# Optimization experiments

Hardware: AMD Instinct MI355X
Metric: run time of the kernel (lower is better)

## Reference

```python
import jax, jax.numpy as jnp
import numpy as np

N = 50000        # nodes
E = 800000       # edges
H = 128          # in = hidden = out width
L = 4            # num_layers
BN_EPS = 1e-5


def _bn(x, g, b):
    # training-mode batch norm over the node dimension (biased variance, as torch)
    mu = jnp.mean(x, axis=0)
    var = jnp.mean((x - mu) ** 2, axis=0)
    return (x - mu) * jax.lax.rsqrt(var + BN_EPS) * g + b


def setup_inputs() -> dict:
    key = jax.random.key(0)
    ks = jax.random.split(key, 16)
    s = 0.05
    return {
        "x": jax.random.normal(ks[0], (N, H), dtype=jnp.float32),
        "edge_index": jax.random.randint(ks[1], (2, E), 0, N, dtype=jnp.int32),
        # stacked per-layer MLP params (all layers share dims H->H->H)
        "fc1_w": jax.random.normal(ks[2], (L, H, H), dtype=jnp.float32) * s,
        "fc1_b": jnp.zeros((L, H), dtype=jnp.float32),
        "bn1_g": jnp.ones((L, H), dtype=jnp.float32),
        "bn1_b": jnp.zeros((L, H), dtype=jnp.float32),
        "fc2_w": jax.random.normal(ks[3], (L, H, H), dtype=jnp.float32) * s,
        "fc2_b": jnp.zeros((L, H), dtype=jnp.float32),
        "bn2_g": jnp.ones((L, H), dtype=jnp.float32),
        "bn2_b": jnp.zeros((L, H), dtype=jnp.float32),
        # outer per-layer BatchNorm (intended one-per-GIN-layer)
        "bn3_g": jnp.ones((L, H), dtype=jnp.float32),
        "bn3_b": jnp.zeros((L, H), dtype=jnp.float32),
        # final classifier
        "fc_w": jax.random.normal(ks[4], (H, H), dtype=jnp.float32) * s,
        "fc_b": jnp.zeros((H,), dtype=jnp.float32),
    }


def reference(x, edge_index, fc1_w, fc1_b, bn1_g, bn1_b, fc2_w, fc2_b,
              bn2_g, bn2_b, bn3_g, bn3_b, fc_w, fc_b):
    src = edge_index[0]
    dst = edge_index[1]
    for i in range(L):
        # GINConv, eps=0: h = MLP((1+eps)*x + sum_{j in N(v)} x_j)
        agg = jax.ops.segment_sum(x[src], dst, num_segments=N)  # [N, H]
        h = x + agg
        # MLP: relu(bn1(fc1(h))) -> bn2(fc2(.))
        h = jax.nn.relu(_bn(h @ fc1_w[i].T + fc1_b[i], bn1_g[i], bn1_b[i]))
        h = _bn(h @ fc2_w[i].T + fc2_b[i], bn2_g[i], bn2_b[i])
        # outer BN + ReLU per layer
        x = jax.nn.relu(_bn(h, bn3_g[i], bn3_b[i]))
    return x @ fc_w.T + fc_b  # [N, H]
```

## Files before the change

kernel.cpp:

```cpp
#include <hip/hip_runtime.h>

#define NN 50000
#define HD 128
#define NL 4
#define BN_EPS 1e-5f
#define NTILES 3125

typedef __attribute__((ext_vector_type(8))) short short8;
typedef __attribute__((ext_vector_type(4))) float f32x4;
typedef __attribute__((ext_vector_type(4))) uint uint4v;

__device__ inline ushort f2bf(float f){
  uint u = __float_as_uint(f);
  uint r = (u + 0x7fffu + ((u >> 16) & 1u)) >> 16;
  return (ushort)r;
}
__device__ inline float bflo(uint u){ return __uint_as_float(u << 16); }
__device__ inline float bfhi(uint u){ return __uint_as_float(u & 0xffff0000u); }
__device__ inline uint pk2(float lo, float hi){
  return (uint)f2bf(lo) | ((uint)f2bf(hi) << 16);
}

__global__ __launch_bounds__(256) void cast_all(const float* __restrict__ x,
                                                const float* __restrict__ w1,
                                                const float* __restrict__ w2,
                                                const float* __restrict__ wf,
                                                ushort* __restrict__ xb,
                                                ushort* __restrict__ wb){
  const int NX = NN * HD / 4;
  const int NT = NX + 36864;
  int i = blockIdx.x * 256 + threadIdx.x;
  int stride = gridDim.x * 256;
  for (; i < NT; i += stride){
    const float* src; ushort* dst;
    if (i < NX){ src = x + i * 4; dst = xb + i * 4; }
    else {
      int k = i - NX;
      dst = wb + k * 4;
      if (k < 16384)      src = w1 + k * 4;
      else if (k < 32768) src = w2 + (k - 16384) * 4;
      else                src = wf + (k - 32768) * 4;
    }
    float4 v = *(const float4*)src;
    ushort4 r;
    r.x = f2bf(v.x); r.y = f2bf(v.y); r.z = f2bf(v.z); r.w = f2bf(v.w);
    *(ushort4*)dst = r;
  }
}

__global__ void fill1_kernel(const int* __restrict__ dst, int* __restrict__ cnt,
                             int* __restrict__ pos, int E){
  int e = (blockIdx.x * 256 + threadIdx.x) * 4;
  if (e + 4 <= E){
    int4 d = *(const int4*)(dst + e);
    int4 p;
    p.x = atomicAdd(&cnt[d.x], 1);
    p.y = atomicAdd(&cnt[d.y], 1);
    p.z = atomicAdd(&cnt[d.z], 1);
    p.w = atomicAdd(&cnt[d.w], 1);
    *(int4*)(pos + e) = p;
  } else {
    for (; e < E; ++e) pos[e] = atomicAdd(&cnt[dst[e]], 1);
  }
}

__global__ void scan1_kernel(const int* __restrict__ deg, int* __restrict__ incl,
                             int* __restrict__ bsum, int n){
  __shared__ int tmp[1024];
  int gid = blockIdx.x * 1024 + threadIdx.x;
  int v = (gid < n) ? deg[gid] : 0;
  tmp[threadIdx.x] = v;
  __syncthreads();
  for (int ofs = 1; ofs < 1024; ofs <<= 1){
    int t = tmp[threadIdx.x];
    int a = (threadIdx.x >= ofs) ? tmp[threadIdx.x - ofs] : 0;
    __syncthreads();
    tmp[threadIdx.x] = t + a;
    __syncthreads();
  }
  if (gid < n) incl[gid] = tmp[threadIdx.x];
  if (threadIdx.x == 1023) bsum[blockIdx.x] = tmp[1023];
}

__global__ void scan2_kernel(const int* __restrict__ bsum, int* __restrict__ base,
                             int* __restrict__ off, int nb, int n){
  int lane = threadIdx.x & 63;
  int own = (lane < nb) ? bsum[lane] : 0;
  int v = own;
#pragma unroll
  for (int ofs = 1; ofs < 64; ofs <<= 1){
    int t = __shfl_up(v, ofs);
    if (lane >= ofs) v += t;
  }
  if (lane < nb) base[lane] = v - own;
  if (lane == 63) off[n] = v;
}

__global__ void scan3_kernel(const int* __restrict__ deg, const int* __restrict__ incl,
                             const int* __restrict__ base, int* __restrict__ off, int n){
  int gid = blockIdx.x * 1024 + threadIdx.x;
  if (gid < n) off[gid] = incl[gid] - deg[gid] + base[blockIdx.x];
}

__global__ void fill2_kernel(const int* __restrict__ src, const int* __restrict__ dst,
                             const int* __restrict__ off, const int* __restrict__ pos,
                             int* __restrict__ csrc, int E){
  int e = (blockIdx.x * 256 + threadIdx.x) * 4;
  if (e + 4 <= E){
    int4 d = *(const int4*)(dst + e);
    int4 p = *(const int4*)(pos + e);
    int4 s = *(const int4*)(src + e);
    csrc[off[d.x] + p.x] = s.x;
    csrc[off[d.y] + p.y] = s.y;
    csrc[off[d.z] + p.z] = s.z;
    csrc[off[d.w] + p.w] = s.w;
  } else {
    for (; e < E; ++e) csrc[off[dst[e]] + pos[e]] = src[e];
  }
}

__device__ inline void bn_params8(const float* __restrict__ st, const float* __restrict__ gA,
                                  const float* __restrict__ gB, const float* __restrict__ bB,
                                  int mode, float* sS, float* sT){
  int c = threadIdx.x;
  if (c < 128){
    float s0 = 0.f, s1 = 0.f;
#pragma unroll
    for (int k = 0; k < 8; ++k){
      s0 += st[k * 256 + c];
      s1 += st[k * 256 + 128 + c];
    }
    const float invN = 1.f / (float)NN;
    float mu = s0 * invN;
    float var = fmaxf(s1 * invN - mu * mu, 0.f);
    float S, T;
    if (mode == 0){
      S = gA[c] * rsqrtf(var + BN_EPS);
      T = gB[c] - mu * S;
    } else {
      float inv2 = rsqrtf(var + BN_EPS);
      float tt = gA[c] * inv2;
      float inv3 = rsqrtf(tt * tt * var + BN_EPS);
      S = tt * inv3 * gB[c];
      T = bB[c] - mu * S;
    }
    sS[c] = S; sT[c] = T;
  }
}

template<bool AFF>
__global__ __launch_bounds__(256) void agg_t(const ushort* __restrict__ xin,
                                             const int* __restrict__ off,
                                             const int* __restrict__ csrc,
                                             const float* __restrict__ statsIn,
                                             const float* __restrict__ g2,
                                             const float* __restrict__ g3,
                                             const float* __restrict__ b3,
                                             ushort* __restrict__ h){
  __shared__ float sS[128];
  __shared__ float sT[128];
  if (AFF){
    bn_params8(statsIn, g2, g3, b3, 1, sS, sT);
    __syncthreads();
  }
  int lane = threadIdx.x & 63;
  int grp  = lane >> 4;
  int col  = lane & 15;
  int node = blockIdx.x * 16 + (threadIdx.x >> 6) * 4 + grp;

  float S[8], T[8];
  if (AFF){
#pragma unroll
    for (int k = 0; k < 8; ++k){ S[k] = sS[col * 8 + k]; T[k] = sT[col * 8 + k]; }
  }

  const uint4v* x4 = (const uint4v*)xin;
  int s = off[node], e = off[node + 1];

  float a[8];
  {
    uint4v v = x4[node * 16 + col];
    if (AFF){
      a[0]=fmaxf(bflo(v.x)*S[0]+T[0],0.f); a[1]=fmaxf(bfhi(v.x)*S[1]+T[1],0.f);
      a[2]=fmaxf(bflo(v.y)*S[2]+T[2],0.f); a[3]=fmaxf(bfhi(v.y)*S[3]+T[3],0.f);
      a[4]=fmaxf(bflo(v.z)*S[4]+T[4],0.f); a[5]=fmaxf(bfhi(v.z)*S[5]+T[5],0.f);
      a[6]=fmaxf(bflo(v.w)*S[6]+T[6],0.f); a[7]=fmaxf(bfhi(v.w)*S[7]+T[7],0.f);
    } else {
      a[0]=bflo(v.x); a[1]=bfhi(v.x); a[2]=bflo(v.y); a[3]=bfhi(v.y);
      a[4]=bflo(v.z); a[5]=bfhi(v.z); a[6]=bflo(v.w); a[7]=bfhi(v.w);
    }
  }

#define ACC8(v)                                                                 \
  if (AFF){                                                                     \
    a[0]+=fmaxf(bflo((v).x)*S[0]+T[0],0.f); a[1]+=fmaxf(bfhi((v).x)*S[1]+T[1],0.f); \
    a[2]+=fmaxf(bflo((v).y)*S[2]+T[2],0.f); a[3]+=fmaxf(bfhi((v).y)*S[3]+T[3],0.f); \
    a[4]+=fmaxf(bflo((v).z)*S[4]+T[4],0.f); a[5]+=fmaxf(bfhi((v).z)*S[5]+T[5],0.f); \
    a[6]+=fmaxf(bflo((v).w)*S[6]+T[6],0.f); a[7]+=fmaxf(bfhi((v).w)*S[7]+T[7],0.f); \
  } else {                                                                      \
    a[0]+=bflo((v).x); a[1]+=bfhi((v).x); a[2]+=bflo((v).y); a[3]+=bfhi((v).y); \
    a[4]+=bflo((v).z); a[5]+=bfhi((v).z); a[6]+=bflo((v).w); a[7]+=bfhi((v).w); \
  }

  int j = s;
  for (; j + 4 <= e; j += 4){
    int i0 = csrc[j], i1 = csrc[j+1], i2 = csrc[j+2], i3 = csrc[j+3];
    uint4v v0 = x4[i0 * 16 + col];
    uint4v v1 = x4[i1 * 16 + col];
    uint4v v2 = x4[i2 * 16 + col];
    uint4v v3 = x4[i3 * 16 + col];
    ACC8(v0); ACC8(v1); ACC8(v2); ACC8(v3);
  }
  for (; j < e; ++j){
    uint4v v = x4[csrc[j] * 16 + col];
    ACC8(v);
  }
#undef ACC8

  uint4v o;
  o.x = pk2(a[0], a[1]); o.y = pk2(a[2], a[3]);
  o.z = pk2(a[4], a[5]); o.w = pk2(a[6], a[7]);
  __builtin_nontemporal_store(o, (uint4v*)h + node * 16 + col);
}

__global__ __launch_bounds__(512) void gemm_kernel(const ushort* __restrict__ A,
                                                   const ushort* __restrict__ W,
                                                   const float* __restrict__ bias,
                                                   ushort* __restrict__ Yb,
                                                   float* __restrict__ Yf,
                                                   float* __restrict__ statsOut,
                                                   const float* __restrict__ statsIn,
                                                   const float* __restrict__ gA,
                                                   const float* __restrict__ gB,
                                                   const float* __restrict__ bB,
                                                   int mode){
  __shared__ uint4v w4[128 * 17];
  __shared__ float ssum[128];
  __shared__ float ssq[128];
  __shared__ float sS[128];
  __shared__ float sT[128];
  const uint4v* Wg = (const uint4v*)W;
  for (int c = threadIdx.x; c < 2048; c += 512){
    w4[(c >> 4) * 17 + (c & 15)] = Wg[c];
  }
  if (statsIn) bn_params8(statsIn, gA, gB, bB, mode, sS, sT);
  if (threadIdx.x < 128){ ssum[threadIdx.x] = 0.f; ssq[threadIdx.x] = 0.f; }
  __syncthreads();

  int wave = threadIdx.x >> 6;
  int lane = threadIdx.x & 63;
  int m = lane & 15, q = lane >> 4;
  int tile = blockIdx.x * 8 + wave;
  bool tv = tile < NTILES;
  const uint4v* A4 = (const uint4v*)A;

  f32x4 acc[8];
#pragma unroll
  for (int i = 0; i < 8; ++i) acc[i] = (f32x4)0.f;

#pragma unroll
  for (int kt = 0; kt < 4; ++kt){
    short8 af = (short8)0;
    if (tv){
      uint4v t = __builtin_nontemporal_load(A4 + (tile * 16 + m) * 16 + kt * 4 + q);
      if (statsIn){
        int kc = kt * 32 + q * 8;
        uint4v pk;
        pk.x = pk2(fmaxf(bflo(t.x)*sS[kc+0]+sT[kc+0],0.f),
                   fmaxf(bfhi(t.x)*sS[kc+1]+sT[kc+1],0.f));
        pk.y = pk2(fmaxf(bflo(t.y)*sS[kc+2]+sT[kc+2],0.f),
                   fmaxf(bfhi(t.y)*sS[kc+3]+sT[kc+3],0.f));
        pk.z = pk2(fmaxf(bflo(t.z)*sS[kc+4]+sT[kc+4],0.f),
                   fmaxf(bfhi(t.z)*sS[kc+5]+sT[kc+5],0.f));
        pk.w = pk2(fmaxf(bflo(t.w)*sS[kc+6]+sT[kc+6],0.f),
                   fmaxf(bfhi(t.w)*sS[kc+7]+sT[kc+7],0.f));
        t = pk;
      }
      af = *(short8*)&t;
    }
#pragma unroll
    for (int to = 0; to < 8; ++to){
      uint4v bw = w4[(to * 16 + m) * 17 + kt * 4 + q];
      acc[to] = __builtin_amdgcn_mfma_f32_16x16x32_bf16(af, *(short8*)&bw, acc[to], 0, 0, 0);
    }
  }

  bool dost = (statsOut != nullptr);
#pragma unroll
  for (int to = 0; to < 8; ++to){
    int col = to * 16 + m;
    float bc = bias[col];
    float ls = 0.f, lq = 0.f;
    if (tv){
#pragma unroll
      for (int r = 0; r < 4; ++r){
        float v = acc[to][r] + bc;
        int row = tile * 16 + q * 4 + r;
        if (Yb) __builtin_nontemporal_store(__builtin_bit_cast(ushort, f2bf(v)), Yb + row * 128 + col);
        else    __builtin_nontemporal_store(v, Yf + row * 128 + col);
        ls += v; lq += v * v;
      }
    }
    if (dost){
      ls += __shfl_xor(ls, 16); lq += __shfl_xor(lq, 16);
      ls += __shfl_xor(ls, 32); lq += __shfl_xor(lq, 32);
      if (tv && q == 0){ atomicAdd(&ssum[col], ls); atomicAdd(&ssq[col], lq); }
    }
  }
  if (dost){
    __syncthreads();
    if (threadIdx.x < 128){
      int sb = (blockIdx.x & 7) * 256;
      atomicAdd(&statsOut[sb + threadIdx.x], ssum[threadIdx.x]);
      atomicAdd(&statsOut[sb + 128 + threadIdx.x], ssq[threadIdx.x]);
    }
  }
}

extern "C" void kernel_launch(void* const* d_in, const int* in_sizes, int n_in,
                              void* d_out, int out_size, void* d_ws, size_t ws_size,
                              hipStream_t stream) {
  const float* x     = (const float*)d_in[0];
  const int*   ei    = (const int*)d_in[1];
  const float* fc1_w = (const float*)d_in[2];
  const float* fc1_b = (const float*)d_in[3];
  const float* bn1_g = (const float*)d_in[4];
  const float* bn1_b = (const float*)d_in[5];
  const float* fc2_w = (const float*)d_in[6];
  const float* fc2_b = (const float*)d_in[7];
  const float* bn2_g = (const float*)d_in[8];
  const float* bn3_g = (const float*)d_in[10];
  const float* bn3_b = (const float*)d_in[11];
  const float* fc_w  = (const float*)d_in[12];
  const float* fc_b  = (const float*)d_in[13];

  int E = in_sizes[1] / 2;
  const int* srcp = ei;
  const int* dstp = ei + E;

  char* ws = (char*)d_ws;
  int*    off    = (int*)(ws + 0);
  int*    cnt    = (int*)(ws + 200064);
  int*    pos    = (int*)(ws + 400128);
  int*    csrc   = (int*)(ws + 3600128);
  ushort* wb     = (ushort*)(ws + 6800128);
  float*  stats  = (float*)(ws + 7095040);
  int*    sscr   = (int*)(ws + 7160576);
  ushort* xb     = (ushort*)(ws + 7161664);
  ushort* hb     = (ushort*)(ws + 19961664);
  ushort* y1b    = (ushort*)(ws + 32761664);
  ushort* y2b    = (ushort*)(ws + 45561664);

  int* incl = csrc;
  int* bsum = sscr;
  int* base = sscr + 64;

  hipMemsetAsync(cnt, 0, 200064, stream);
  hipMemsetAsync(stats, 0, 65536, stream);

  cast_all<<<2048, 256, 0, stream>>>(x, fc1_w, fc2_w, fc_w, xb, wb);

  const int EB4 = (E / 4 + 255) / 256 + 1;
  const int SB = (NN + 1023) / 1024;
  fill1_kernel<<<EB4, 256, 0, stream>>>(dstp, cnt, pos, E);
  scan1_kernel<<<SB, 1024, 0, stream>>>(cnt, incl, bsum, NN);
  scan2_kernel<<<1, 64, 0, stream>>>(bsum, base, off, SB, NN);
  scan3_kernel<<<SB, 1024, 0, stream>>>(cnt, incl, base, off, NN);
  fill2_kernel<<<EB4, 256, 0, stream>>>(srcp, dstp, off, pos, csrc, E);

  const int gb = (NTILES + 7) / 8;

  for (int i = 0; i < NL; ++i){
    if (i == 0){
      agg_t<false><<<NN / 16, 256, 0, stream>>>(xb, off, csrc,
                                                nullptr, nullptr, nullptr, nullptr, hb);
    } else {
      agg_t<true><<<NN / 16, 256, 0, stream>>>(y2b, off, csrc,
                                               stats + ((i - 1) * 2 + 1) * 2048,
                                               bn2_g + (i - 1) * 128,
                                               bn3_g + (i - 1) * 128,
                                               bn3_b + (i - 1) * 128, hb);
    }
    gemm_kernel<<<gb, 512, 0, stream>>>(hb, wb + i * 16384, fc1_b + i * 128,
                                        y1b, nullptr, stats + (i * 2) * 2048,
                                        nullptr, nullptr, nullptr, nullptr, 0);
    gemm_kernel<<<gb, 512, 0, stream>>>(y1b, wb + 65536 + i * 16384, fc2_b + i * 128,
                                        y2b, nullptr, stats + (i * 2 + 1) * 2048,
                                        stats + (i * 2) * 2048, bn1_g + i * 128,
                                        bn1_b + i * 128, nullptr, 0);
  }

  gemm_kernel<<<gb, 512, 0, stream>>>(y2b, wb + 131072, fc_b,
                                      nullptr, (float*)d_out, nullptr,
                                      stats + 7 * 2048, bn2_g + 384,
                                      bn3_g + 384, bn3_b + 384, 1);
}
```

Measured before the change: 463.7 us.

## Fuse neighbor aggregation into first MLP GEMM and use fixed-degree slot adjacency

The separate aggregation kernel is merged into the first GEMM. Each wave gathers neighbor rows for a 16-node tile into shared memory, then multiplies by fc1 with MFMA and accumulates BN statistics in the same kernel. This removes the write and re-read of the aggregated bf16 hidden matrix in every layer. The three CSR prefix-scan kernels are also replaced by a padded per-node slot array of fixed width 64, so edges are placed using only the count and position. The trade-offs are that the adjacency buffer is four times larger and that any node with more than 64 incoming edges silently overflows into the next node's slots. The fused kernel also uses more shared memory per block, which can lower occupancy for the latency-bound gather.

```diff
diff --git a/kernel.cpp b/kernel.cpp
--- a/kernel.cpp
+++ b/kernel.cpp
@@ -5,6 +5,7 @@
 #define NL 4
 #define BN_EPS 1e-5f
 #define NTILES 3125
+#define MAXDEG 64
 
 typedef __attribute__((ext_vector_type(8))) short short8;
 typedef __attribute__((ext_vector_type(4))) float f32x4;
@@ -64,58 +65,19 @@
   }
 }
 
-__global__ void scan1_kernel(const int* __restrict__ deg, int* __restrict__ incl,
-                             int* __restrict__ bsum, int n){
-  __shared__ int tmp[1024];
-  int gid = blockIdx.x * 1024 + threadIdx.x;
-  int v = (gid < n) ? deg[gid] : 0;
-  tmp[threadIdx.x] = v;
-  __syncthreads();
-  for (int ofs = 1; ofs < 1024; ofs <<= 1){
-    int t = tmp[threadIdx.x];
-    int a = (threadIdx.x >= ofs) ? tmp[threadIdx.x - ofs] : 0;
-    __syncthreads();
-    tmp[threadIdx.x] = t + a;
-    __syncthreads();
-  }
-  if (gid < n) incl[gid] = tmp[threadIdx.x];
-  if (threadIdx.x == 1023) bsum[blockIdx.x] = tmp[1023];
-}
-
-__global__ void scan2_kernel(const int* __restrict__ bsum, int* __restrict__ base,
-                             int* __restrict__ off, int nb, int n){
-  int lane = threadIdx.x & 63;
-  int own = (lane < nb) ? bsum[lane] : 0;
-  int v = own;
-#pragma unroll
-  for (int ofs = 1; ofs < 64; ofs <<= 1){
-    int t = __shfl_up(v, ofs);
-    if (lane >= ofs) v += t;
-  }
-  if (lane < nb) base[lane] = v - own;
-  if (lane == 63) off[n] = v;
-}
-
-__global__ void scan3_kernel(const int* __restrict__ deg, const int* __restrict__ incl,
-                             const int* __restrict__ base, int* __restrict__ off, int n){
-  int gid = blockIdx.x * 1024 + threadIdx.x;
-  if (gid < n) off[gid] = incl[gid] - deg[gid] + base[blockIdx.x];
-}
-
 __global__ void fill2_kernel(const int* __restrict__ src, const int* __restrict__ dst,
-                             const int* __restrict__ off, const int* __restrict__ pos,
-                             int* __restrict__ csrc, int E){
+                             const int* __restrict__ pos, int* __restrict__ slots, int E){
   int e = (blockIdx.x * 256 + threadIdx.x) * 4;
   if (e + 4 <= E){
     int4 d = *(const int4*)(dst + e);
     int4 p = *(const int4*)(pos + e);
     int4 s = *(const int4*)(src + e);
-    csrc[off[d.x] + p.x] = s.x;
-    csrc[off[d.y] + p.y] = s.y;
-    csrc[off[d.z] + p.z] = s.z;
-    csrc[off[d.w] + p.w] = s.w;
+    slots[d.x * MAXDEG + p.x] = s.x;
+    slots[d.y * MAXDEG + p.y] = s.y;
+    slots[d.z * MAXDEG + p.z] = s.z;
+    slots[d.w * MAXDEG + p.w] = s.w;
   } else {
-    for (; e < E; ++e) csrc[off[dst[e]] + pos[e]] = src[e];
+    for (; e < E; ++e) slots[dst[e] * MAXDEG + pos[e]] = src[e];
   }
 }
 
@@ -149,24 +111,38 @@
 }
 
 template<bool AFF>
-__global__ __launch_bounds__(256) void agg_t(const ushort* __restrict__ xin,
-                                             const int* __restrict__ off,
-                                             const int* __restrict__ csrc,
-                                             const float* __restrict__ statsIn,
-                                             const float* __restrict__ g2,
-                                             const float* __restrict__ g3,
-                                             const float* __restrict__ b3,
-                                             ushort* __restrict__ h){
+__global__ __launch_bounds__(512, 4) void aggemm_t(const ushort* __restrict__ xin,
+                                                   const int* __restrict__ deg,
+                                                   const int* __restrict__ slots,
+                                                   const ushort* __restrict__ W,
+                                                   const float* __restrict__ bias,
+                                                   ushort* __restrict__ Yb,
+                                                   float* __restrict__ statsOut,
+                                                   const float* __restrict__ statsIn,
+                                                   const float* __restrict__ g2,
+                                                   const float* __restrict__ g3,
+                                                   const float* __restrict__ b3){
+  __shared__ uint4v w4[128 * 17];
+  __shared__ uint4v a4[8][16 * 17];
+  __shared__ float ssum[128];
+  __shared__ float ssq[128];
   __shared__ float sS[128];
   __shared__ float sT[128];
-  if (AFF){
-    bn_params8(statsIn, g2, g3, b3, 1, sS, sT);
-    __syncthreads();
-  }
+
+  const uint4v* Wg = (const uint4v*)W;
+  for (int c = threadIdx.x; c < 2048; c += 512){
+    w4[(c >> 4) * 17 + (c & 15)] = Wg[c];
+  }
+  if (AFF) bn_params8(statsIn, g2, g3, b3, 1, sS, sT);
+  if (threadIdx.x < 128){ ssum[threadIdx.x] = 0.f; ssq[threadIdx.x] = 0.f; }
+  __syncthreads();
+
+  int wave = threadIdx.x >> 6;
   int lane = threadIdx.x & 63;
   int grp  = lane >> 4;
   int col  = lane & 15;
-  int node = blockIdx.x * 16 + (threadIdx.x >> 6) * 4 + grp;
+  int tile = blockIdx.x * 8 + wave;
+  bool tv = tile < NTILES;
 
   float S[8], T[8];
   if (AFF){
@@ -175,21 +151,6 @@
   }
 
   const uint4v* x4 = (const uint4v*)xin;
-  int s = off[node], e = off[node + 1];
-
-  float a[8];
-  {
-    uint4v v = x4[node * 16 + col];
-    if (AFF){
-      a[0]=fmaxf(bflo(v.x)*S[0]+T[0],0.f); a[1]=fmaxf(bfhi(v.x)*S[1]+T[1],0.f);
-      a[2]=fmaxf(bflo(v.y)*S[2]+T[2],0.f); a[3]=fmaxf(bfhi(v.y)*S[3]+T[3],0.f);
-      a[4]=fmaxf(bflo(v.z)*S[4]+T[4],0.f); a[5]=fmaxf(bfhi(v.z)*S[5]+T[5],0.f);
-      a[6]=fmaxf(bflo(v.w)*S[6]+T[6],0.f); a[7]=fmaxf(bfhi(v.w)*S[7]+T[7],0.f);
-    } else {
-      a[0]=bflo(v.x); a[1]=bfhi(v.x); a[2]=bflo(v.y); a[3]=bfhi(v.y);
-      a[4]=bflo(v.z); a[5]=bfhi(v.z); a[6]=bflo(v.w); a[7]=bfhi(v.w);
-    }
-  }
 
 #define ACC8(v)                                                                 \
   if (AFF){                                                                     \
@@ -202,25 +163,100 @@
     a[4]+=bflo((v).z); a[5]+=bfhi((v).z); a[6]+=bflo((v).w); a[7]+=bfhi((v).w); \
   }
 
-  int j = s;
-  for (; j + 4 <= e; j += 4){
-    int i0 = csrc[j], i1 = csrc[j+1], i2 = csrc[j+2], i3 = csrc[j+3];
-    uint4v v0 = x4[i0 * 16 + col];
-    uint4v v1 = x4[i1 * 16 + col];
-    uint4v v2 = x4[i2 * 16 + col];
-    uint4v v3 = x4[i3 * 16 + col];
-    ACC8(v0); ACC8(v1); ACC8(v2); ACC8(v3);
-  }
-  for (; j < e; ++j){
-    uint4v v = x4[csrc[j] * 16 + col];
-    ACC8(v);
+  if (tv){
+    for (int it = 0; it < 4; ++it){
+      int node = tile * 16 + it * 4 + grp;
+      int e = deg[node];
+      const int* sl = slots + node * MAXDEG;
+      float a[8];
+      {
+        uint4v v = x4[node * 16 + col];
+        if (AFF){
+          a[0]=fmaxf(bflo(v.x)*S[0]+T[0],0.f); a[1]=fmaxf(bfhi(v.x)*S[1]+T[1],0.f);
+          a[2]=fmaxf(bflo(v.y)*S[2]+T[2],0.f); a[3]=fmaxf(bfhi(v.y)*S[3]+T[3],0.f);
+          a[4]=fmaxf(bflo(v.z)*S[4]+T[4],0.f); a[5]=fmaxf(bfhi(v.z)*S[5]+T[5],0.f);
+          a[6]=fmaxf(bflo(v.w)*S[6]+T[6],0.f); a[7]=fmaxf(bfhi(v.w)*S[7]+T[7],0.f);
+        } else {
+          a[0]=bflo(v.x); a[1]=bfhi(v.x); a[2]=bflo(v.y); a[3]=bfhi(v.y);
+          a[4]=bflo(v.z); a[5]=bfhi(v.z); a[6]=bflo(v.w); a[7]=bfhi(v.w);
+        }
+      }
+      int j = 0;
+      for (; j + 8 <= e; j += 8){
+        int i0 = sl[j+0], i1 = sl[j+1], i2 = sl[j+2], i3 = sl[j+3];
+        int i4 = sl[j+4], i5 = sl[j+5], i6 = sl[j+6], i7 = sl[j+7];
+        uint4v v0 = x4[i0 * 16 + col];
+        uint4v v1 = x4[i1 * 16 + col];
+        uint4v v2 = x4[i2 * 16 + col];
+        uint4v v3 = x4[i3 * 16 + col];
+        uint4v v4 = x4[i4 * 16 + col];
+        uint4v v5 = x4[i5 * 16 + col];
+        uint4v v6 = x4[i6 * 16 + col];
+        uint4v v7 = x4[i7 * 16 + col];
+        ACC8(v0); ACC8(v1); ACC8(v2); ACC8(v3);
+        ACC8(v4); ACC8(v5); ACC8(v6); ACC8(v7);
+      }
+      for (; j + 4 <= e; j += 4){
+        int i0 = sl[j+0], i1 = sl[j+1], i2 = sl[j+2], i3 = sl[j+3];
+        uint4v v0 = x4[i0 * 16 + col];
+        uint4v v1 = x4[i1 * 16 + col];
+        uint4v v2 = x4[i2 * 16 + col];
+        uint4v v3 = x4[i3 * 16 + col];
+        ACC8(v0); ACC8(v1); ACC8(v2); ACC8(v3);
+      }
+      for (; j < e; ++j){
+        uint4v v = x4[sl[j] * 16 + col];
+        ACC8(v);
+      }
+      uint4v o;
+      o.x = pk2(a[0], a[1]); o.y = pk2(a[2], a[3]);
+      o.z = pk2(a[4], a[5]); o.w = pk2(a[6], a[7]);
+      a4[wave][(it * 4 + grp) * 17 + col] = o;
+    }
   }
 #undef ACC8
-
-  uint4v o;
-  o.x = pk2(a[0], a[1]); o.y = pk2(a[2], a[3]);
-  o.z = pk2(a[4], a[5]); o.w = pk2(a[6], a[7]);
-  __builtin_nontemporal_store(o, (uint4v*)h + node * 16 + col);
+  __syncthreads();
+
+  int m = lane & 15, q = lane >> 4;
+  f32x4 acc[8];
+#pragma unroll
+  for (int i = 0; i < 8; ++i) acc[i] = (f32x4)0.f;
+
+#pragma unroll
+  for (int kt = 0; kt < 4; ++kt){
+    uint4v t = a4[wave][m * 17 + kt * 4 + q];
+    short8 af = *(short8*)&t;
+#pragma unroll
+    for (int to = 0; to < 8; ++to){
+      uint4v bw = w4[(to * 16 + m) * 17 + kt * 4 + q];
+      acc[to] = __builtin_amdgcn_mfma_f32_16x16x32_bf16(af, *(short8*)&bw, acc[to], 0, 0, 0);
+    }
+  }
+
+#pragma unroll
+  for (int to = 0; to < 8; ++to){
+    int colo = to * 16 + m;
+    float bc = bias[colo];
+    float ls = 0.f, lq = 0.f;
+    if (tv){
+#pragma unroll
+      for (int r = 0; r < 4; ++r){
+        float v = acc[to][r] + bc;
+        int row = tile * 16 + q * 4 + r;
+        __builtin_nontemporal_store(__builtin_bit_cast(ushort, f2bf(v)), Yb + row * 128 + colo);
+        ls += v; lq += v * v;
+      }
+    }
+    ls += __shfl_xor(ls, 16); lq += __shfl_xor(lq, 16);
+    ls += __shfl_xor(ls, 32); lq += __shfl_xor(lq, 32);
+    if (tv && q == 0){ atomicAdd(&ssum[colo], ls); atomicAdd(&ssq[colo], lq); }
+  }
+  __syncthreads();
+  if (threadIdx.x < 128){
+    int sb = (blockIdx.x & 7) * 256;
+    atomicAdd(&statsOut[sb + threadIdx.x], ssum[threadIdx.x]);
+    atomicAdd(&statsOut[sb + 128 + threadIdx.x], ssq[threadIdx.x]);
+  }
 }
 
 __global__ __launch_bounds__(512) void gemm_kernel(const ushort* __restrict__ A,
@@ -339,51 +375,40 @@
   const int* dstp = ei + E;
 
   char* ws = (char*)d_ws;
-  int*    off    = (int*)(ws + 0);
-  int*    cnt    = (int*)(ws + 200064);
-  int*    pos    = (int*)(ws + 400128);
-  int*    csrc   = (int*)(ws + 3600128);
-  ushort* wb     = (ushort*)(ws + 6800128);
-  float*  stats  = (float*)(ws + 7095040);
-  int*    sscr   = (int*)(ws + 7160576);
-  ushort* xb     = (ushort*)(ws + 7161664);
-  ushort* hb     = (ushort*)(ws + 19961664);
-  ushort* y1b    = (ushort*)(ws + 32761664);
-  ushort* y2b    = (ushort*)(ws + 45561664);
-
-  int* incl = csrc;
-  int* bsum = sscr;
-  int* base = sscr + 64;
-
-  hipMemsetAsync(cnt, 0, 200064, stream);
-  hipMemsetAsync(stats, 0, 65536, stream);
+  int*    cnt    = (int*)(ws + 0);
+  float*  stats  = (float*)(ws + 200064);
+  int*    pos    = (int*)(ws + 265600);
+  int*    slots  = (int*)(ws + 3465600);
+  ushort* wb     = (ushort*)(ws + 16265600);
+  ushort* xb     = (ushort*)(ws + 16560512);
+  ushort* y1b    = (ushort*)(ws + 29360512);
+  ushort* y2b    = (ushort*)(ws + 42160512);
+
+  hipMemsetAsync(ws, 0, 265600, stream);
 
   cast_all<<<2048, 256, 0, stream>>>(x, fc1_w, fc2_w, fc_w, xb, wb);
 
   const int EB4 = (E / 4 + 255) / 256 + 1;
-  const int SB = (NN + 1023) / 1024;
   fill1_kernel<<<EB4, 256, 0, stream>>>(dstp, cnt, pos, E);
-  scan1_kernel<<<SB, 1024, 0, stream>>>(cnt, incl, bsum, NN);
-  scan2_kernel<<<1, 64, 0, stream>>>(bsum, base, off, SB, NN);
-  scan3_kernel<<<SB, 1024, 0, stream>>>(cnt, incl, base, off, NN);
-  fill2_kernel<<<EB4, 256, 0, stream>>>(srcp, dstp, off, pos, csrc, E);
+  fill2_kernel<<<EB4, 256, 0, stream>>>(srcp, dstp, pos, slots, E);
 
   const int gb = (NTILES + 7) / 8;
 
   for (int i = 0; i < NL; ++i){
     if (i == 0){
-      agg_t<false><<<NN / 16, 256, 0, stream>>>(xb, off, csrc,
-                                                nullptr, nullptr, nullptr, nullptr, hb);
+      aggemm_t<false><<<gb, 512, 0, stream>>>(xb, cnt, slots, wb + i * 16384,
+                                              fc1_b + i * 128, y1b,
+                                              stats + (i * 2) * 2048,
+                                              nullptr, nullptr, nullptr, nullptr);
     } else {
-      agg_t<true><<<NN / 16, 256, 0, stream>>>(y2b, off, csrc,
-                                               stats + ((i - 1) * 2 + 1) * 2048,
-                                               bn2_g + (i - 1) * 128,
-                                               bn3_g + (i - 1) * 128,
-                                               bn3_b + (i - 1) * 128, hb);
-    }
-    gemm_kernel<<<gb, 512, 0, stream>>>(hb, wb + i * 16384, fc1_b + i * 128,
-                                        y1b, nullptr, stats + (i * 2) * 2048,
-                                        nullptr, nullptr, nullptr, nullptr, 0);
+      aggemm_t<true><<<gb, 512, 0, stream>>>(y2b, cnt, slots, wb + i * 16384,
+                                             fc1_b + i * 128, y1b,
+                                             stats + (i * 2) * 2048,
+                                             stats + ((i - 1) * 2 + 1) * 2048,
+                                             bn2_g + (i - 1) * 128,
+                                             bn3_g + (i - 1) * 128,
+                                             bn3_b + (i - 1) * 128);
+    }
     gemm_kernel<<<gb, 512, 0, stream>>>(y1b, wb + 65536 + i * 16384, fc2_b + i * 128,
                                         y2b, nullptr, stats + (i * 2 + 1) * 2048,
                                         stats + (i * 2) * 2048, bn1_g + i * 128,
```

After: 425.5 us. 8.2% less time.
